# Kernel optimization log

Measured on AMD Instinct MI355X. Metric: run time of the kernel, lower is better.

Reference implementation:

```python
import jax, jax.numpy as jnp
import numpy as np

B, T, D, K = 64, 4096, 128, 512

def setup_inputs() -> dict:
    key = jax.random.key(0)
    k1, k2, k3 = jax.random.split(key, 3)
    embeddings = jax.random.normal(k1, (B, T, D), dtype=jnp.float32)
    mask = jax.random.bernoulli(k2, 0.9, (B, T))
    W = jax.random.normal(k3, (D,), dtype=jnp.float32) * (1.0 / np.sqrt(D))
    b = jnp.zeros((1,), dtype=jnp.float32)
    return {"embeddings": embeddings, "mask": mask, "k": K, "W": W, "b": b}

def reference(embeddings, mask, k, W, b):
    batch, T, dim = embeddings.shape
    if k >= T:
        return embeddings, mask
    # linear score head: (B,T,D) @ (D,) + b -> (B,T)
    scores = jnp.einsum("btd,d->bt", embeddings, W) + b[0]
    neg_inf = jnp.array(-jnp.inf, dtype=scores.dtype)
    scores = jnp.where(mask, scores, neg_inf)
    soft_scores = jax.nn.sigmoid(scores)  # sigmoid(-inf) == 0
    _, topk_idx = jax.lax.top_k(scores, k)          # (B, k)
    topk_idx_sorted = jnp.sort(topk_idx, axis=1)    # preserve original token order
    rows = jnp.arange(batch)[:, None]
    hard_mask = jnp.zeros_like(scores).at[rows, topk_idx].set(1.0)
    # straight-through estimator: hard forward, soft gradient
    ste_mask = hard_mask - jax.lax.stop_gradient(soft_scores) + soft_scores
    weighted = embeddings * ste_mask[:, :, None]
    selected = jnp.take_along_axis(weighted, topk_idx_sorted[:, :, None], axis=1)  # (B,k,D)
    selected_mask = jnp.take_along_axis(mask, topk_idx_sorted, axis=1)             # (B,k)
    return selected, selected_mask
```

## Files before the change

kernel.cpp:

```cpp
#include <hip/hip_runtime.h>
#include <hip/hip_bf16.h>

#define BB 64
#define TT 4096
#define DD 128
#define KK 512

#define KEY_NEG_INF 0x007FFFFFu

__global__ __launch_bounds__(256) void k_scores(
    const float* __restrict__ emb, const int* __restrict__ mask,
    const float* __restrict__ W, const float* __restrict__ bias,
    unsigned int* __restrict__ keys_out)
{
    const int wave = threadIdx.x >> 6;
    const int lane = threadIdx.x & 63;
    const int half = lane >> 5;
    const int sub  = lane & 31;
    const int pair0 = (blockIdx.x * 4 + wave) * 8;

    const float4 w = ((const float4*)W)[sub];
    const double w0 = (double)w.x, w1 = (double)w.y, w2 = (double)w.z, w3 = (double)w.w;
    const double b0 = (double)bias[0];

#pragma unroll
    for (int i = 0; i < 8; ++i) {
        const int t = (pair0 + i) * 2 + half;
        const float4 e = ((const float4*)emb)[(size_t)t * 32 + sub];
        double s = (double)e.x * w0 + (double)e.y * w1
                 + (double)e.z * w2 + (double)e.w * w3;
        s += __shfl_xor(s, 16, 64);
        s += __shfl_xor(s,  8, 64);
        s += __shfl_xor(s,  4, 64);
        s += __shfl_xor(s,  2, 64);
        s += __shfl_xor(s,  1, 64);
        if (sub == 0) {
            const float val = (float)(s + b0);
            const unsigned int u = __float_as_uint(val);
            unsigned int key = (u & 0x80000000u) ? ~u : (u | 0x80000000u);
            if (!mask[t]) key = KEY_NEG_INF;
            keys_out[t] = key;
        }
    }
}

__global__ __launch_bounds__(1024) void k_select(
    const unsigned int* __restrict__ keys_in, const int* __restrict__ mask,
    int* __restrict__ idx_out, float* __restrict__ mask_out)
{
    __shared__ unsigned int keys[TT];
    __shared__ unsigned int hist[16][257];
    __shared__ unsigned int hist_final[256];
    __shared__ unsigned int wsum[16];
    __shared__ unsigned int bcast[2];

    const int row  = blockIdx.x;
    const int tid  = threadIdx.x;
    const int wv   = tid >> 6;
    const int lane = tid & 63;
    const unsigned int* krow = keys_in + (size_t)row * TT;
    const int*          mrow = mask    + (size_t)row * TT;

    const uint4 kv = ((const uint4*)krow)[tid];
    ((uint4*)keys)[tid] = kv;

    unsigned int prefix = 0;
    unsigned int count_above = 0;
    for (int pass = 0; pass < 4; ++pass) {
        const int shift = 24 - 8 * pass;
        for (int i = tid; i < 16 * 257; i += 1024) ((unsigned int*)hist)[i] = 0;
        __syncthreads();
#pragma unroll
        for (int i = 0; i < 4; ++i) {
            const unsigned int k = keys[tid * 4 + i];
            const bool in_group = (pass == 0) || ((k >> (shift + 8)) == prefix);
            if (in_group) atomicAdd(&hist[wv][(k >> shift) & 0xFFu], 1u);
        }
        __syncthreads();
        if (tid < 256) {
            unsigned int s = 0;
#pragma unroll
            for (int w = 0; w < 16; ++w) s += hist[w][tid];
            hist_final[tid] = s;
        }
        __syncthreads();
        if (wv == 0) {
            unsigned int v[4], c[4];
            unsigned int run = 0;
#pragma unroll
            for (int j = 0; j < 4; ++j) {
                v[j] = hist_final[255 - (4 * lane + j)];
                run += v[j];
                c[j] = run;
            }
            unsigned int scan = run;
#pragma unroll
            for (int off = 1; off < 64; off <<= 1) {
                const unsigned int u = __shfl_up(scan, off, 64);
                if (lane >= off) scan += u;
            }
            const unsigned int excl_w = scan - run;
#pragma unroll
            for (int j = 0; j < 4; ++j) {
                const unsigned int incl = excl_w + c[j];
                const unsigned int excl = incl - v[j];
                if (count_above + incl >= KK && count_above + excl < KK) {
                    bcast[0] = 255u - (unsigned int)(4 * lane + j);
                    bcast[1] = count_above + excl;
                }
            }
        }
        __syncthreads();
        prefix = (prefix << 8) | bcast[0];
        count_above = bcast[1];
    }
    const unsigned int vstar = prefix;
    const unsigned int need  = KK - count_above;

    unsigned int gt = 0, eq = 0;
#pragma unroll
    for (int i = 0; i < 4; ++i) {
        const unsigned int k = keys[tid * 4 + i];
        gt += (k > vstar);
        eq += (k == vstar);
    }
    unsigned int packed = (gt << 16) | eq;
    unsigned int scan = packed;
#pragma unroll
    for (int off = 1; off < 64; off <<= 1) {
        const unsigned int u = __shfl_up(scan, off, 64);
        if (lane >= off) scan += u;
    }
    if (lane == 63) wsum[wv] = scan;
    __syncthreads();
    unsigned int add = 0;
    for (int w = 0; w < wv; ++w) add += wsum[w];
    const unsigned int before = scan - packed + add;
    unsigned int gt_b = before >> 16;
    unsigned int eq_b = before & 0xFFFFu;
#pragma unroll
    for (int i = 0; i < 4; ++i) {
        const int t = tid * 4 + i;
        const unsigned int k = keys[t];
        if (k > vstar) {
            const unsigned int pos = gt_b + (eq_b < need ? eq_b : need);
            idx_out[row * KK + pos]  = t;
            mask_out[row * KK + pos] = mrow[t] ? 1.0f : 0.0f;
            gt_b++;
        } else if (k == vstar) {
            if (eq_b < need) {
                const unsigned int pos = gt_b + eq_b;
                idx_out[row * KK + pos]  = t;
                mask_out[row * KK + pos] = mrow[t] ? 1.0f : 0.0f;
            }
            eq_b++;
        }
    }
}

__global__ __launch_bounds__(256) void k_gather(
    const float* __restrict__ emb, const int* __restrict__ idx,
    float* __restrict__ out)
{
    const int gp   = blockIdx.x * 8 + (threadIdx.x >> 5);
    const int lane = threadIdx.x & 31;
    const int b = gp >> 9;
    const int t = idx[gp];
    const float4* src = (const float4*)(emb + ((size_t)b * TT + t) * DD);
    float4*       dst = (float4*)(out + (size_t)gp * DD);
    dst[lane] = src[lane];
}

extern "C" void kernel_launch(void* const* d_in, const int* in_sizes, int n_in,
                              void* d_out, int out_size, void* d_ws, size_t ws_size,
                              hipStream_t stream)
{
    const float* emb  = (const float*)d_in[0];
    const int*   mask = (const int*)d_in[1];
    const float* W    = (const float*)d_in[3];
    const float* bias = (const float*)d_in[4];

    float* out_sel  = (float*)d_out;
    float* out_mask = (float*)d_out + (size_t)BB * KK * DD;

    unsigned int* keys = (unsigned int*)d_ws;
    int*          idx  = (int*)((char*)d_ws + (size_t)BB * TT * sizeof(unsigned int));

    k_scores<<<BB * TT / 64, 256, 0, stream>>>(emb, mask, W, bias, keys);
    k_select<<<BB, 1024, 0, stream>>>(keys, mask, idx, out_mask);
    k_gather<<<BB * KK / 8, 256, 0, stream>>>(emb, idx, out_sel);
}
```

Measured before the change: 212.9 us.

## Fuse gather into select kernel and stage score keys through shared memory

```diff
diff --git a/kernel.cpp b/kernel.cpp
--- a/kernel.cpp
+++ b/kernel.cpp
@@ -13,19 +13,23 @@
     const float* __restrict__ W, const float* __restrict__ bias,
     unsigned int* __restrict__ keys_out)
 {
-    const int wave = threadIdx.x >> 6;
-    const int lane = threadIdx.x & 63;
+    __shared__ unsigned int skeys[256];
+
+    const int tid  = threadIdx.x;
+    const int wave = tid >> 6;
+    const int lane = tid & 63;
     const int half = lane >> 5;
     const int sub  = lane & 31;
-    const int pair0 = (blockIdx.x * 4 + wave) * 8;
+    const int t0_block = blockIdx.x * 256;
+    const int t0_wave  = t0_block + wave * 64;
 
     const float4 w = ((const float4*)W)[sub];
     const double w0 = (double)w.x, w1 = (double)w.y, w2 = (double)w.z, w3 = (double)w.w;
     const double b0 = (double)bias[0];
 
-#pragma unroll
-    for (int i = 0; i < 8; ++i) {
-        const int t = (pair0 + i) * 2 + half;
+#pragma unroll 8
+    for (int i = 0; i < 32; ++i) {
+        const int t = t0_wave + 2 * i + half;
         const float4 e = ((const float4*)emb)[(size_t)t * 32 + sub];
         double s = (double)e.x * w0 + (double)e.y * w1
                  + (double)e.z * w2 + (double)e.w * w3;
@@ -37,22 +41,27 @@
         if (sub == 0) {
             const float val = (float)(s + b0);
             const unsigned int u = __float_as_uint(val);
-            unsigned int key = (u & 0x80000000u) ? ~u : (u | 0x80000000u);
-            if (!mask[t]) key = KEY_NEG_INF;
-            keys_out[t] = key;
+            skeys[wave * 64 + 2 * i + half] = (u & 0x80000000u) ? ~u : (u | 0x80000000u);
         }
     }
+    __syncthreads();
+    const int t = t0_block + tid;
+    unsigned int key = skeys[tid];
+    if (!mask[t]) key = KEY_NEG_INF;
+    keys_out[t] = key;
 }
 
-__global__ __launch_bounds__(1024) void k_select(
+__global__ __launch_bounds__(1024) void k_selgath(
     const unsigned int* __restrict__ keys_in, const int* __restrict__ mask,
-    int* __restrict__ idx_out, float* __restrict__ mask_out)
+    const float* __restrict__ emb,
+    float* __restrict__ out_sel, float* __restrict__ mask_out)
 {
     __shared__ unsigned int keys[TT];
     __shared__ unsigned int hist[16][257];
     __shared__ unsigned int hist_final[256];
     __shared__ unsigned int wsum[16];
     __shared__ unsigned int bcast[2];
+    __shared__ int idx_l[KK];
 
     const int row  = blockIdx.x;
     const int tid  = threadIdx.x;
@@ -144,31 +153,28 @@
         const unsigned int k = keys[t];
         if (k > vstar) {
             const unsigned int pos = gt_b + (eq_b < need ? eq_b : need);
-            idx_out[row * KK + pos]  = t;
+            idx_l[pos] = t;
             mask_out[row * KK + pos] = mrow[t] ? 1.0f : 0.0f;
             gt_b++;
         } else if (k == vstar) {
             if (eq_b < need) {
                 const unsigned int pos = gt_b + eq_b;
-                idx_out[row * KK + pos]  = t;
+                idx_l[pos] = t;
                 mask_out[row * KK + pos] = mrow[t] ? 1.0f : 0.0f;
             }
             eq_b++;
         }
     }
-}
+    __syncthreads();
 
-__global__ __launch_bounds__(256) void k_gather(
-    const float* __restrict__ emb, const int* __restrict__ idx,
-    float* __restrict__ out)
-{
-    const int gp   = blockIdx.x * 8 + (threadIdx.x >> 5);
-    const int lane = threadIdx.x & 31;
-    const int b = gp >> 9;
-    const int t = idx[gp];
-    const float4* src = (const float4*)(emb + ((size_t)b * TT + t) * DD);
-    float4*       dst = (float4*)(out + (size_t)gp * DD);
-    dst[lane] = src[lane];
+    const int half = lane >> 5;
+    const int sub  = lane & 31;
+    for (int jj = wv * 2; jj < KK; jj += 32) {
+        const int j = jj + half;
+        const int t = idx_l[j];
+        const float4 v = ((const float4*)(emb + ((size_t)row * TT + t) * DD))[sub];
+        ((float4*)(out_sel + ((size_t)row * KK + j) * DD))[sub] = v;
+    }
 }
 
 extern "C" void kernel_launch(void* const* d_in, const int* in_sizes, int n_in,
@@ -184,9 +190,7 @@
     float* out_mask = (float*)d_out + (size_t)BB * KK * DD;
 
     unsigned int* keys = (unsigned int*)d_ws;
-    int*          idx  = (int*)((char*)d_ws + (size_t)BB * TT * sizeof(unsigned int));
 
-    k_scores<<<BB * TT / 64, 256, 0, stream>>>(emb, mask, W, bias, keys);
-    k_select<<<BB, 1024, 0, stream>>>(keys, mask, idx, out_mask);
-    k_gather<<<BB * KK / 8, 256, 0, stream>>>(emb, idx, out_sel);
+    k_scores<<<BB * TT / 256, 256, 0, stream>>>(emb, mask, W, bias, keys);
+    k_selgath<<<BB, 1024, 0, stream>>>(keys, mask, emb, out_sel, out_mask);
 }
```

Measured after the change: 215.7 us. Within noise of the previous version (+1.3%).
